# Optimization experiments

Hardware: AMD Instinct MI355X
Metric: run time of the kernel (lower is better)

## Reference

```python
import jax, jax.numpy as jnp
import numpy as np

B, LQ, LD, H, C = 128, 32, 512, 768, 128


def setup_inputs() -> dict:
    key = jax.random.key(0)
    ks = jax.random.split(key, 8)
    return {
        "query_hidden": jax.random.normal(ks[0], (B, LQ, H), dtype=jnp.float32),
        "doc_hidden": jax.random.normal(ks[1], (B, LD, H), dtype=jnp.float32),
        "query_mask": jax.random.randint(ks[2], (B, LQ), 0, 2, dtype=jnp.int32),
        "doc_mask": jax.random.randint(ks[3], (B, LD), 0, 2, dtype=jnp.int32),
        "W_comp": jax.random.normal(ks[4], (H, C), dtype=jnp.float32) * (1.0 / np.sqrt(H)),
        "b_comp": jax.random.normal(ks[5], (C,), dtype=jnp.float32) * 0.02,
        "w_stop": jax.random.normal(ks[6], (C, 1), dtype=jnp.float32) * (1.0 / np.sqrt(C)),
        "b_stop": jnp.ones((1,), dtype=jnp.float32),  # nn.init.constant_(bias, 1)
        "score_merger": jnp.zeros((1,), dtype=jnp.float32),
    }


def reference(query_hidden, doc_hidden, query_mask, doc_mask,
              W_comp, b_comp, w_stop, b_stop, score_merger):
    qm = query_mask.astype(bool)  # [B, LQ]
    dm = doc_mask.astype(bool)    # [B, LD]

    # encode_shared: CLS vec is the UNcompressed hidden state at position 0
    q_cls = query_hidden[:, 0, :]  # [B, H]
    d_cls = doc_hidden[:, 0, :]    # [B, H]

    # compressor (Linear H->C)
    q_vecs = jnp.einsum('blh,hc->blc', query_hidden, W_comp) + b_comp  # [B, LQ, C]
    d_tok = jnp.einsum('blh,hc->blc', doc_hidden, W_comp) + b_comp     # [B, LD, C]

    # encode_query: zero masked query tokens
    q_vecs = q_vecs * qm[..., None]

    # encode_doc: stopword reducer (relu of Linear C->1), then importance + mask
    importance = jax.nn.relu(jnp.einsum('blc,co->blo', d_tok, w_stop) + b_stop)  # [B, LD, 1]
    d_vecs = d_tok * importance * dm[..., None]

    # CLS score: dot product of (uncompressed) CLS vectors
    cls_score = jnp.sum(q_cls * d_cls, axis=-1)  # [B]

    # term score: MaxSim over doc tokens, masked sum over query tokens
    scores = jnp.einsum('bqc,bkc->bqk', q_vecs, d_vecs)      # [B, LQ, LD]
    scores = jnp.where(dm[:, None, :], scores, -1000.0)
    term = jnp.max(scores, axis=-1)                          # [B, LQ]
    term_score = jnp.sum(jnp.where(qm, term, 0.0), axis=-1)  # [B]

    w = jax.nn.sigmoid(score_merger[0])
    cls_score = cls_score * w
    term_score = term_score * (1.0 - w)
    score = cls_score + term_score
    return (score, cls_score, term_score)
```

## Files before the change

kernel.cpp:

```cpp
#include <hip/hip_runtime.h>
#include <hip/hip_bf16.h>

#define Bb 128
#define LQ 32
#define LD 512
#define Hh 768
#define Cc 128

#define DBLOCKS ((Bb * LD) / 64)
#define QBLOCKS ((Bb * LQ) / 64)

typedef short bf16x8 __attribute__((ext_vector_type(8)));
typedef short bf16x4 __attribute__((ext_vector_type(4)));
typedef float f32x4 __attribute__((ext_vector_type(4)));

__device__ __forceinline__ short f2bf(float f) {
  union { float f; unsigned u; } v;
  v.f = f;
  unsigned u = v.u + (0x7FFFu + ((v.u >> 16) & 1u));
  return (short)(u >> 16);
}

__device__ __forceinline__ float b2f(short s) {
  union { unsigned u; float f; } v;
  v.u = ((unsigned)(unsigned short)s) << 16;
  return v.f;
}

__global__ __launch_bounds__(256) void k_wt(const float* __restrict__ W,
                                            short* __restrict__ Wt) {
  int idx = blockIdx.x * 256 + threadIdx.x;
  int h = idx >> 7;
  int c = idx & 127;
  Wt[c * Hh + h] = f2bf(W[idx]);
}

__global__ __launch_bounds__(256, 4) void k_proj_q(
    const float* __restrict__ qh, const short* __restrict__ Wt,
    const float* __restrict__ bcomp, const int* __restrict__ qmask,
    float* __restrict__ qv) {
  constexpr int ASTR = 144;
  constexpr int BSTR = 160;
  constexpr int ASZ = 64 * ASTR;
  constexpr int BSZ = 128 * BSTR;
  __shared__ __align__(16) char sm[ASZ + BSZ];

  const int tid = threadIdx.x;
  const int w = tid >> 6;
  const int lane = tid & 63;
  const int quad = lane >> 4;
  const int lm = lane & 15;

  const long row0b = (long)blockIdx.x * 64;

  const float* gA = qh + (row0b + w * 16 + (lane >> 4)) * (long)Hh + (lane & 15) * 4;
  const short* gB = Wt + (w * 32 + (lane >> 3)) * Hh + (lane & 7) * 8;
  const int aoff = (w * 16 + (lane >> 4)) * ASTR + (lane & 15) * 8;
  const int boff = (w * 32 + (lane >> 3)) * BSTR + (lane & 7) * 16;

  char* bufA = sm;
  char* bufB = sm + ASZ;

  f32x4 acc[8];
#pragma unroll
  for (int j = 0; j < 8; ++j) acc[j] = (f32x4){0.f, 0.f, 0.f, 0.f};

  float4 ar[4];
  bf16x8 br[4];
#pragma unroll
  for (int i = 0; i < 4; ++i) ar[i] = *(const float4*)(gA + i * 4 * Hh);
#pragma unroll
  for (int i = 0; i < 4; ++i) br[i] = *(const bf16x8*)(gB + i * 8 * Hh);

  for (int kk = 0; kk < Hh / 64; ++kk) {
    __syncthreads();
#pragma unroll
    for (int i = 0; i < 4; ++i) {
      bf16x4 p;
      p[0] = f2bf(ar[i].x); p[1] = f2bf(ar[i].y);
      p[2] = f2bf(ar[i].z); p[3] = f2bf(ar[i].w);
      *(bf16x4*)(bufA + aoff + i * 4 * ASTR) = p;
    }
#pragma unroll
    for (int i = 0; i < 4; ++i)
      *(bf16x8*)(bufB + boff + i * 8 * BSTR) = br[i];
    __syncthreads();

    {
      const long go = (kk + 1 < Hh / 64) ? (long)(kk + 1) * 64 : 0;
#pragma unroll
      for (int i = 0; i < 4; ++i) ar[i] = *(const float4*)(gA + i * 4 * Hh + go);
#pragma unroll
      for (int i = 0; i < 4; ++i) br[i] = *(const bf16x8*)(gB + i * 8 * Hh + go);
    }

#pragma unroll
    for (int ks = 0; ks < 2; ++ks) {
      bf16x8 fa = *(const bf16x8*)(bufA + (w * 16 + lm) * ASTR + ks * 64 + quad * 16);
#pragma unroll
      for (int j = 0; j < 8; ++j) {
        bf16x8 fb = *(const bf16x8*)(bufB + (j * 16 + lm) * BSTR + ks * 64 + quad * 16);
        acc[j] = __builtin_amdgcn_mfma_f32_16x16x32_bf16(fa, fb, acc[j], 0, 0, 0);
      }
    }
  }

  const long row0 = row0b + w * 16;
  float bc[8];
#pragma unroll
  for (int j = 0; j < 8; ++j) bc[j] = bcomp[j * 16 + lm];

#pragma unroll
  for (int r = 0; r < 4; ++r) {
    const long row = row0 + quad * 4 + r;
    const float scale = (float)qmask[row];
    float* yr = qv + row * Cc;
#pragma unroll
    for (int j = 0; j < 8; ++j) yr[j * 16 + lm] = (acc[j][r] + bc[j]) * scale;
  }
}

__global__ __launch_bounds__(256, 4) void k_fused(
    const float* __restrict__ dh, const short* __restrict__ Wt,
    const float* __restrict__ qv, const float* __restrict__ bcomp,
    const int* __restrict__ dmask, const float* __restrict__ wstop,
    const float* __restrict__ bstop, float* __restrict__ partial) {
  constexpr int ASTR = 144;
  constexpr int SSTR = 136;
  constexpr int NK = Hh / 64;
  __shared__ __align__(16) char smem[26112 + 256 + 512];

  char* bufA = smem;
  short* dvt = (short*)smem;
  short* lqt = (short*)(smem + 17408);
  int* dmsk = (int*)(smem + 26112);
  float* pm = (float*)(smem + 26112 + 256);

  const int tid = threadIdx.x;
  const int w = tid >> 6;
  const int lane = tid & 63;
  const int quad = lane >> 4;
  const int lm = lane & 15;

  const int b = blockIdx.x >> 3;
  const int chunk = blockIdx.x & 7;
  const long row0b = (long)b * LD + chunk * 64;

  if (tid < 64) dmsk[tid] = dmask[row0b + tid];

  const float* gA = dh + (row0b + w * 16 + (lane >> 4)) * (long)Hh + (lane & 15) * 4;
  const short* gB = Wt + lm * Hh + quad * 8;
  const int aoff = (w * 16 + (lane >> 4)) * ASTR + (lane & 15) * 8;

  f32x4 acc[8];
#pragma unroll
  for (int j = 0; j < 8; ++j) acc[j] = (f32x4){0.f, 0.f, 0.f, 0.f};

  float4 arA[4], arB[4];
#pragma unroll
  for (int i = 0; i < 4; ++i) arA[i] = *(const float4*)(gA + i * 4 * Hh);
#pragma unroll
  for (int i = 0; i < 4; ++i) arB[i] = *(const float4*)(gA + 64 + i * 4 * Hh);

  auto iter = [&](int kk, float4 (&ar)[4]) {
#pragma unroll
    for (int i = 0; i < 4; ++i) {
      bf16x4 p;
      p[0] = f2bf(ar[i].x); p[1] = f2bf(ar[i].y);
      p[2] = f2bf(ar[i].z); p[3] = f2bf(ar[i].w);
      *(bf16x4*)(bufA + aoff + i * 4 * ASTR) = p;
    }
#pragma unroll
    for (int ks = 0; ks < 2; ++ks) {
      bf16x8 fa = *(const bf16x8*)(bufA + (w * 16 + lm) * ASTR + ks * 64 + quad * 16);
      bf16x8 fbv[8];
#pragma unroll
      for (int j = 0; j < 8; ++j)
        fbv[j] = *(const bf16x8*)(gB + j * 16 * Hh + kk * 64 + ks * 32);
#pragma unroll
      for (int j = 0; j < 8; ++j)
        acc[j] = __builtin_amdgcn_mfma_f32_16x16x32_bf16(fa, fbv[j], acc[j], 0, 0, 0);
    }
    const long go = (kk + 2 < NK) ? (long)(kk + 2) * 64 : 0;
#pragma unroll
    for (int i = 0; i < 4; ++i)
      ar[i] = *(const float4*)(gA + go + i * 4 * Hh);
  };

  for (int kp = 0; kp < NK / 2; ++kp) {
    iter(2 * kp, arA);
    iter(2 * kp + 1, arB);
  }

  __syncthreads();

  {
    const float4* src = (const float4*)(qv + (size_t)b * LQ * Cc);
    float4 t[4];
#pragma unroll
    for (int k = 0; k < 4; ++k) t[k] = src[tid + k * 256];
#pragma unroll
    for (int k = 0; k < 4; ++k) {
      const int i = tid + k * 256;
      const int q = i >> 5;
      const int c = (i & 31) << 2;
      bf16x4 p;
      p[0] = f2bf(t[k].x); p[1] = f2bf(t[k].y);
      p[2] = f2bf(t[k].z); p[3] = f2bf(t[k].w);
      *(bf16x4*)&lqt[q * SSTR + c] = p;
    }
  }

  float bc[8], wsv[8];
#pragma unroll
  for (int j = 0; j < 8; ++j) bc[j] = bcomp[j * 16 + lm];
#pragma unroll
  for (int j = 0; j < 8; ++j) wsv[j] = wstop[j * 16 + lm];
  const float bs = bstop[0];

#pragma unroll
  for (int r = 0; r < 4; ++r) {
    const int lrow = w * 16 + quad * 4 + r;
    float v[8];
#pragma unroll
    for (int j = 0; j < 8; ++j) v[j] = acc[j][r] + bc[j];
    float p = 0.f;
#pragma unroll
    for (int j = 0; j < 8; ++j) p += v[j] * wsv[j];
    p += __shfl_xor(p, 1);
    p += __shfl_xor(p, 2);
    p += __shfl_xor(p, 4);
    p += __shfl_xor(p, 8);
    const float imp = fmaxf(p + bs, 0.f);
    const float scale = imp * (float)dmsk[lrow];
#pragma unroll
    for (int j = 0; j < 8; ++j)
      dvt[lrow * SSTR + j * 16 + lm] = f2bf(v[j] * scale);
  }
  __syncthreads();

  const int qt = tid & 15;
  const int kt = tid >> 4;
  const int kbase = kt * 4;
  float a[2][4];
#pragma unroll
  for (int qi = 0; qi < 2; ++qi)
#pragma unroll
    for (int ki = 0; ki < 4; ++ki) a[qi][ki] = 0.f;

  for (int c = 0; c < Cc; c += 8) {
    bf16x8 q0 = *(const bf16x8*)&lqt[qt * SSTR + c];
    bf16x8 q1 = *(const bf16x8*)&lqt[(qt + 16) * SSTR + c];
    bf16x8 d0 = *(const bf16x8*)&dvt[(kbase + 0) * SSTR + c];
    bf16x8 d1 = *(const bf16x8*)&dvt[(kbase + 1) * SSTR + c];
    bf16x8 d2 = *(const bf16x8*)&dvt[(kbase + 2) * SSTR + c];
    bf16x8 d3 = *(const bf16x8*)&dvt[(kbase + 3) * SSTR + c];
#pragma unroll
    for (int e = 0; e < 8; ++e) {
      const float f0 = b2f(q0[e]);
      const float f1 = b2f(q1[e]);
      const float g0 = b2f(d0[e]);
      const float g1 = b2f(d1[e]);
      const float g2 = b2f(d2[e]);
      const float g3 = b2f(d3[e]);
      a[0][0] += f0 * g0; a[0][1] += f0 * g1;
      a[0][2] += f0 * g2; a[0][3] += f0 * g3;
      a[1][0] += f1 * g0; a[1][1] += f1 * g1;
      a[1][2] += f1 * g2; a[1][3] += f1 * g3;
    }
  }
  float m0 = -1000.f, m1 = -1000.f;
#pragma unroll
  for (int ki = 0; ki < 4; ++ki) {
    if (dmsk[kbase + ki]) {
      m0 = fmaxf(m0, a[0][ki]);
      m1 = fmaxf(m1, a[1][ki]);
    }
  }
  m0 = fmaxf(m0, __shfl_xor(m0, 16));
  m0 = fmaxf(m0, __shfl_xor(m0, 32));
  m1 = fmaxf(m1, __shfl_xor(m1, 16));
  m1 = fmaxf(m1, __shfl_xor(m1, 32));
  if (lane < 16) {
    pm[w * 32 + lane] = m0;
    pm[w * 32 + lane + 16] = m1;
  }
  __syncthreads();
  if (tid < LQ) {
    float mx = fmaxf(fmaxf(pm[tid], pm[32 + tid]),
                     fmaxf(pm[64 + tid], pm[96 + tid]));
    partial[((size_t)b * LQ + tid) * 8 + chunk] = mx;
  }
}

__global__ __launch_bounds__(256) void k_final(
    const float* __restrict__ qh, const float* __restrict__ dh,
    const int* __restrict__ qmask, const float* __restrict__ partial,
    const float* __restrict__ merger, float* __restrict__ out) {
  const int b = blockIdx.x;
  const int tid = threadIdx.x;
  __shared__ float red[256];
  __shared__ float clss;
  const float* qc = qh + (size_t)b * LQ * Hh;
  const float* dc = dh + (size_t)b * LD * Hh;
  float s = 0.f;
  for (int h = tid; h < Hh; h += 256) s += qc[h] * dc[h];
  red[tid] = s;
  __syncthreads();
  for (int off = 128; off > 0; off >>= 1) {
    if (tid < off) red[tid] += red[tid + off];
    __syncthreads();
  }
  if (tid == 0) clss = red[0];
  __syncthreads();
  float t = 0.f;
  if (tid < LQ) {
    const float* pp = partial + ((size_t)b * LQ + tid) * 8;
    float mx = pp[0];
#pragma unroll
    for (int c = 1; c < 8; ++c) mx = fmaxf(mx, pp[c]);
    if (qmask[b * LQ + tid]) t = mx;
  }
  red[tid] = t;
  __syncthreads();
  for (int off = 128; off > 0; off >>= 1) {
    if (tid < off) red[tid] += red[tid + off];
    __syncthreads();
  }
  if (tid == 0) {
    float w = 1.f / (1.f + expf(-merger[0]));
    float cs = clss * w;
    float ts = red[0] * (1.f - w);
    out[b] = cs + ts;
    out[Bb + b] = cs;
    out[2 * Bb + b] = ts;
  }
}

extern "C" void kernel_launch(void* const* d_in, const int* in_sizes, int n_in,
                              void* d_out, int out_size, void* d_ws, size_t ws_size,
                              hipStream_t stream) {
  const float* qh  = (const float*)d_in[0];
  const float* dh  = (const float*)d_in[1];
  const int*   qm  = (const int*)d_in[2];
  const int*   dm  = (const int*)d_in[3];
  const float* W   = (const float*)d_in[4];
  const float* bc  = (const float*)d_in[5];
  const float* wst = (const float*)d_in[6];
  const float* bst = (const float*)d_in[7];
  const float* mrg = (const float*)d_in[8];
  float* out = (float*)d_out;

  char* ws = (char*)d_ws;
  short* Wt  = (short*)ws;
  float* qv  = (float*)(ws + 196608);
  float* prt = (float*)(ws + 196608 + 2097152);

  k_wt<<<(Hh * Cc) / 256, 256, 0, stream>>>(W, Wt);
  k_proj_q<<<QBLOCKS, 256, 0, stream>>>(qh, Wt, bc, qm, qv);
  k_fused<<<DBLOCKS, 256, 0, stream>>>(dh, Wt, qv, bc, dm, wst, bst, prt);
  k_final<<<Bb, 256, 0, stream>>>(qh, dh, qm, prt, mrg, out);
}
```

Measured before the change: 388.4 us.

## Stage weight tiles through shared memory and single-buffer the doc GEMM loop

The doc projection kernel now loads each 128x64 bf16 weight tile cooperatively into LDS once per K-step, instead of having every wave read 8 B fragments straight from global memory. The A register double-buffer is replaced by one register prefetch of both A and B. Each K-step now has two barriers, and the occupancy hint rises to 5 blocks per CU. The aim is to cut redundant global/L2 traffic for the weights, at the cost of more LDS use and extra synchronisation.

```diff
diff --git a/kernel.cpp b/kernel.cpp
--- a/kernel.cpp
+++ b/kernel.cpp
@@ -120,21 +120,24 @@
   }
 }
 
-__global__ __launch_bounds__(256, 4) void k_fused(
+__global__ __launch_bounds__(256, 5) void k_doc(
     const float* __restrict__ dh, const short* __restrict__ Wt,
     const float* __restrict__ qv, const float* __restrict__ bcomp,
     const int* __restrict__ dmask, const float* __restrict__ wstop,
     const float* __restrict__ bstop, float* __restrict__ partial) {
   constexpr int ASTR = 144;
+  constexpr int BSTR = 160;
+  constexpr int ASZ = 64 * ASTR;
   constexpr int SSTR = 136;
   constexpr int NK = Hh / 64;
-  __shared__ __align__(16) char smem[26112 + 256 + 512];
+  __shared__ __align__(16) char smem[29696 + 256 + 512];
 
   char* bufA = smem;
+  char* bufB = smem + ASZ;
   short* dvt = (short*)smem;
   short* lqt = (short*)(smem + 17408);
-  int* dmsk = (int*)(smem + 26112);
-  float* pm = (float*)(smem + 26112 + 256);
+  int* dmsk = (int*)(smem + 29696);
+  float* pm = (float*)(smem + 29696 + 256);
 
   const int tid = threadIdx.x;
   const int w = tid >> 6;
@@ -149,20 +152,23 @@
   if (tid < 64) dmsk[tid] = dmask[row0b + tid];
 
   const float* gA = dh + (row0b + w * 16 + (lane >> 4)) * (long)Hh + (lane & 15) * 4;
-  const short* gB = Wt + lm * Hh + quad * 8;
+  const short* gB = Wt + (w * 32 + (lane >> 3)) * Hh + (lane & 7) * 8;
   const int aoff = (w * 16 + (lane >> 4)) * ASTR + (lane & 15) * 8;
+  const int boff = (w * 32 + (lane >> 3)) * BSTR + (lane & 7) * 16;
 
   f32x4 acc[8];
 #pragma unroll
   for (int j = 0; j < 8; ++j) acc[j] = (f32x4){0.f, 0.f, 0.f, 0.f};
 
-  float4 arA[4], arB[4];
-#pragma unroll
-  for (int i = 0; i < 4; ++i) arA[i] = *(const float4*)(gA + i * 4 * Hh);
-#pragma unroll
-  for (int i = 0; i < 4; ++i) arB[i] = *(const float4*)(gA + 64 + i * 4 * Hh);
-
-  auto iter = [&](int kk, float4 (&ar)[4]) {
+  float4 ar[4];
+  bf16x8 br[4];
+#pragma unroll
+  for (int i = 0; i < 4; ++i) ar[i] = *(const float4*)(gA + i * 4 * Hh);
+#pragma unroll
+  for (int i = 0; i < 4; ++i) br[i] = *(const bf16x8*)(gB + i * 8 * Hh);
+
+  for (int kk = 0; kk < NK; ++kk) {
+    __syncthreads();
 #pragma unroll
     for (int i = 0; i < 4; ++i) {
       bf16x4 p;
@@ -171,25 +177,27 @@
       *(bf16x4*)(bufA + aoff + i * 4 * ASTR) = p;
     }
 #pragma unroll
+    for (int i = 0; i < 4; ++i)
+      *(bf16x8*)(bufB + boff + i * 8 * BSTR) = br[i];
+    __syncthreads();
+
+    {
+      const long go = (kk + 1 < NK) ? (long)(kk + 1) * 64 : 0;
+#pragma unroll
+      for (int i = 0; i < 4; ++i) ar[i] = *(const float4*)(gA + i * 4 * Hh + go);
+#pragma unroll
+      for (int i = 0; i < 4; ++i) br[i] = *(const bf16x8*)(gB + i * 8 * Hh + go);
+    }
+
+#pragma unroll
     for (int ks = 0; ks < 2; ++ks) {
       bf16x8 fa = *(const bf16x8*)(bufA + (w * 16 + lm) * ASTR + ks * 64 + quad * 16);
-      bf16x8 fbv[8];
-#pragma unroll
-      for (int j = 0; j < 8; ++j)
-        fbv[j] = *(const bf16x8*)(gB + j * 16 * Hh + kk * 64 + ks * 32);
-#pragma unroll
-      for (int j = 0; j < 8; ++j)
-        acc[j] = __builtin_amdgcn_mfma_f32_16x16x32_bf16(fa, fbv[j], acc[j], 0, 0, 0);
-    }
-    const long go = (kk + 2 < NK) ? (long)(kk + 2) * 64 : 0;
-#pragma unroll
-    for (int i = 0; i < 4; ++i)
-      ar[i] = *(const float4*)(gA + go + i * 4 * Hh);
-  };
-
-  for (int kp = 0; kp < NK / 2; ++kp) {
-    iter(2 * kp, arA);
-    iter(2 * kp + 1, arB);
+#pragma unroll
+      for (int j = 0; j < 8; ++j) {
+        bf16x8 fb = *(const bf16x8*)(bufB + (j * 16 + lm) * BSTR + ks * 64 + quad * 16);
+        acc[j] = __builtin_amdgcn_mfma_f32_16x16x32_bf16(fa, fb, acc[j], 0, 0, 0);
+      }
+    }
   }
 
   __syncthreads();
@@ -358,6 +366,6 @@
 
   k_wt<<<(Hh * Cc) / 256, 256, 0, stream>>>(W, Wt);
   k_proj_q<<<QBLOCKS, 256, 0, stream>>>(qh, Wt, bc, qm, qv);
-  k_fused<<<DBLOCKS, 256, 0, stream>>>(dh, Wt, qv, bc, dm, wst, bst, prt);
+  k_doc<<<DBLOCKS, 256, 0, stream>>>(dh, Wt, qv, bc, dm, wst, bst, prt);
   k_final<<<Bb, 256, 0, stream>>>(qh, dh, qm, prt, mrg, out);
 }
```

Measured after the change: 326.8 us. 1.19x faster.
